# Optimization experiments

Hardware: AMD Instinct MI355X
Metric: run time of the kernel (lower is better)

The kernel has to match this reference:

```python
import jax, jax.numpy as jnp
import numpy as np

B, T, C = 4, 2048, 2048
N_HEAD = 16
HEAD_DIM = C // N_HEAD
ROPE_BASE = 10000.0


def setup_inputs() -> dict:
    key = jax.random.key(0)
    k1, k2, k3 = jax.random.split(key, 3)
    x = jax.random.normal(k1, (B, T, C), dtype=jnp.float32)
    Wqkv = jax.random.normal(k2, (C, 3 * C), dtype=jnp.float32) * 0.02
    bqkv = jnp.zeros((3 * C,), dtype=jnp.float32)
    Wproj = jax.random.normal(k3, (C, C), dtype=jnp.float32) * 0.02
    bproj = jnp.zeros((C,), dtype=jnp.float32)
    return {"x": x, "Wqkv": Wqkv, "bqkv": bqkv, "Wproj": Wproj, "bproj": bproj}


def _rope_cos_sin(seq_len, head_dim, dtype):
    inv_freq = 1.0 / (ROPE_BASE ** (jnp.arange(0, head_dim, 2, dtype=jnp.float32) / head_dim))
    t = jnp.arange(seq_len, dtype=jnp.float32)
    freqs = jnp.einsum("i,j->ij", t, inv_freq)          # [T, D/2]
    emb = jnp.concatenate([freqs, freqs], axis=-1)       # [T, D]
    return jnp.cos(emb).astype(dtype), jnp.sin(emb).astype(dtype)


def _rotate_half(x):
    half = x.shape[-1] // 2
    x1, x2 = x[..., :half], x[..., half:]
    return jnp.concatenate([-x2, x1], axis=-1)


def reference(x, Wqkv, bqkv, Wproj, bproj):
    b, t, c = x.shape
    qkv = x @ Wqkv + bqkv                                # [B, T, 3C]
    q, k, v = jnp.split(qkv, 3, axis=-1)
    # [B, T, C] -> [B, H, T, D]
    def to_heads(u):
        return u.reshape(b, t, N_HEAD, HEAD_DIM).transpose(0, 2, 1, 3)
    q, k, v = to_heads(q), to_heads(k), to_heads(v)
    cos, sin = _rope_cos_sin(t, HEAD_DIM, x.dtype)       # [T, D]
    cos = cos[None, None]                                # [1, 1, T, D]
    sin = sin[None, None]
    q = q * cos + _rotate_half(q) * sin
    k = k * cos + _rotate_half(k) * sin
    scale = 1.0 / np.sqrt(HEAD_DIM).astype(np.float32)
    scores = jnp.einsum("bhqd,bhkd->bhqk", q, k) * scale  # [B, H, T, T]
    causal = jnp.tril(jnp.ones((t, t), dtype=bool))
    scores = jnp.where(causal[None, None], scores, jnp.finfo(scores.dtype).min)
    att = jax.nn.softmax(scores, axis=-1)
    y = jnp.einsum("bhqk,bhkd->bhqd", att, v)             # [B, H, T, D]
    y = y.transpose(0, 2, 1, 3).reshape(b, t, c)
    return y @ Wproj + bproj
```

## Files before the change

### kernel.cpp

```cpp
#include <hip/hip_runtime.h>
#include <hip/hip_bf16.h>
#include <stdint.h>
#include <math.h>

#define NB 4
#define NT 2048
#define NC 2048
#define NH 16
#define HD 128
#define BT (NB*NT)

typedef __attribute__((ext_vector_type(8))) short s16x8;
typedef __attribute__((ext_vector_type(4))) short s16x4;
typedef __attribute__((ext_vector_type(4))) float f32x4;

typedef __attribute__((address_space(1))) void as1_void;
typedef __attribute__((address_space(3))) void as3_void;

static __device__ __forceinline__ unsigned short f2bf(float f) {
  union { float f; uint32_t u; } v; v.f = f;
  return (unsigned short)((v.u + 0x7fffu + ((v.u >> 16) & 1u)) >> 16);
}
static __device__ __forceinline__ float bf2f(unsigned short u) {
  union { uint32_t u; float f; } v; v.u = ((uint32_t)u) << 16;
  return v.f;
}
static __device__ __forceinline__ void async16(unsigned short* lds, const unsigned short* g) {
  __builtin_amdgcn_global_load_lds((as1_void*)g, (as3_void*)lds, 16, 0, 0);
}
static __device__ __forceinline__ uint32_t lds_off(void* p) {
  return (uint32_t)(size_t)(as3_void*)p;
}

__global__ void k_convert_bf16(const float* __restrict__ in, unsigned short* __restrict__ out, int n8) {
  int i = blockIdx.x * blockDim.x + threadIdx.x;
  if (i >= n8) return;
  const float4* p = (const float4*)in + (size_t)i * 2;
  float4 a = p[0], b = p[1];
  union { unsigned short s[8]; uint4 u; } o;
  o.s[0] = f2bf(a.x); o.s[1] = f2bf(a.y); o.s[2] = f2bf(a.z); o.s[3] = f2bf(a.w);
  o.s[4] = f2bf(b.x); o.s[5] = f2bf(b.y); o.s[6] = f2bf(b.z); o.s[7] = f2bf(b.w);
  ((uint4*)out)[i] = o.u;
}

__global__ void k_transpose_bf16(const float* __restrict__ W, unsigned short* __restrict__ WT, int K, int N) {
  __shared__ unsigned short tile[64][65];
  const int k0 = blockIdx.y * 64, n0 = blockIdx.x * 64;
  const int t = threadIdx.x;
  const int jj = t & 63, base_i = t >> 6;
  #pragma unroll
  for (int p = 0; p < 16; ++p) {
    int i = p * 4 + base_i;
    tile[i][jj] = f2bf(W[(size_t)(k0 + i) * N + n0 + jj]);
  }
  __syncthreads();
  #pragma unroll
  for (int p = 0; p < 16; ++p) {
    int j = p * 4 + base_i;
    WT[(size_t)(n0 + j) * K + k0 + jj] = tile[jj][j];
  }
}

__global__ void k_rope(unsigned short* __restrict__ Q, unsigned short* __restrict__ Kb) {
  int idx = blockIdx.x * 256 + threadIdx.x;
  int d = idx & 63;
  int tpos = (idx >> 6) & (NT - 1);
  int bh = idx >> 17;
  size_t o = ((size_t)bh * NT + tpos) * HD + d;
  float invf = exp2f(-(float)d * 0.2076205059304602f);
  float ang = (float)tpos * invf;
  float s, c;
  __sincosf(ang, &s, &c);
  float q1 = bf2f(Q[o]),  q2 = bf2f(Q[o + 64]);
  float k1 = bf2f(Kb[o]), k2 = bf2f(Kb[o + 64]);
  const float qs = 0.08838834764831845f * 1.4426950408889634f;
  Q[o]       = f2bf((q1 * c - q2 * s) * qs);
  Q[o + 64]  = f2bf((q2 * c + q1 * s) * qs);
  Kb[o]      = f2bf(k1 * c - k2 * s);
  Kb[o + 64] = f2bf(k2 * c + k1 * s);
}

template<int MODE>
__global__ __launch_bounds__(256, 2)
void k_gemm_bt2(const unsigned short* __restrict__ A,
                const unsigned short* __restrict__ Bt,
                const float* __restrict__ bias,
                float* __restrict__ OutF,
                unsigned short* __restrict__ Qd,
                unsigned short* __restrict__ Kd,
                unsigned short* __restrict__ Vd,
                int M, int N, int K)
{
  __shared__ __align__(16) unsigned short Al[256 * 64];
  __shared__ __align__(16) unsigned short Bl[128 * 64];
  const int t = threadIdx.x;
  const int l = t & 63;
  const int wv = t >> 6;
  const int wm = wv >> 1, wn = wv & 1;
  const int bm = blockIdx.y * 256, bn = blockIdx.x * 128;
  const int lr = l & 15, lg = l >> 4;

  f32x4 acc[8][4];
  #pragma unroll
  for (int i = 0; i < 8; ++i)
    #pragma unroll
    for (int j = 0; j < 4; ++j)
      acc[i][j] = f32x4{0.f, 0.f, 0.f, 0.f};

  for (int k0 = 0; k0 < K; k0 += 64) {
    #pragma unroll
    for (int i = 0; i < 8; ++i) {
      const int Cc = i * 256 + t;
      const int row = Cc >> 3;
      const int kc = (Cc & 7) ^ (row & 7);
      async16(&Al[(i * 256 + (t & 192)) * 8], &A[(size_t)(bm + row) * K + k0 + kc * 8]);
    }
    #pragma unroll
    for (int i = 0; i < 4; ++i) {
      const int Cc = i * 256 + t;
      const int row = Cc >> 3;
      const int kc = (Cc & 7) ^ (row & 7);
      async16(&Bl[(i * 256 + (t & 192)) * 8], &Bt[(size_t)(bn + row) * K + k0 + kc * 8]);
    }
    __syncthreads();
    #pragma unroll
    for (int kk = 0; kk < 2; ++kk) {
      s16x8 af[8], bfr[4];
      #pragma unroll
      for (int mi = 0; mi < 8; ++mi) {
        const int row = wm * 128 + mi * 16 + lr;
        const int ch = (kk * 4 + lg) ^ (row & 7);
        af[mi] = *(const s16x8*)&Al[row * 64 + ch * 8];
      }
      #pragma unroll
      for (int ni = 0; ni < 4; ++ni) {
        const int row = wn * 64 + ni * 16 + lr;
        const int ch = (kk * 4 + lg) ^ (row & 7);
        bfr[ni] = *(const s16x8*)&Bl[row * 64 + ch * 8];
      }
      __builtin_amdgcn_s_setprio(1);
      #pragma unroll
      for (int mi = 0; mi < 8; ++mi)
        #pragma unroll
        for (int ni = 0; ni < 4; ++ni)
          acc[mi][ni] = __builtin_amdgcn_mfma_f32_16x16x32_bf16(af[mi], bfr[ni], acc[mi][ni], 0, 0, 0);
      __builtin_amdgcn_s_setprio(0);
    }
    __syncthreads();
  }

  #pragma unroll
  for (int mi = 0; mi < 8; ++mi) {
    #pragma unroll
    for (int ni = 0; ni < 4; ++ni) {
      const int col = bn + wn * 64 + ni * 16 + lr;
      const float bv = bias[col];
      #pragma unroll
      for (int r = 0; r < 4; ++r) {
        const int row = bm + wm * 128 + mi * 16 + lg * 4 + r;
        const float v = acc[mi][ni][r] + bv;
        if (MODE == 1) {
          OutF[(size_t)row * N + col] = v;
        } else {
          const int which = col >> 11;
          const int cc = col & 2047;
          const int h = cc >> 7, d = cc & 127;
          const int b = row >> 11, tp = row & 2047;
          unsigned short* dst = (which == 0) ? Qd : (which == 1 ? Kd : Vd);
          dst[(((size_t)(b * NH + h)) * NT + tp) * HD + d] = f2bf(v);
        }
      }
    }
  }
}

__global__ __launch_bounds__(256, 2)
void k_attn(const unsigned short* __restrict__ Q,
            const unsigned short* __restrict__ Kg,
            const unsigned short* __restrict__ Vg,
            unsigned short* __restrict__ Yatt)
{
  __shared__ __align__(16) unsigned short Kl[2][64 * 128];
  __shared__ __align__(16) unsigned short Vl[2][64 * 128];
  const int bh = blockIdx.x;
  const int pair = blockIdx.y;
  const int b = bh >> 4, h = bh & 15;
  const int t = threadIdx.x, l = t & 63, wv = t >> 6;
  const int lr = l & 15, lg = l >> 4;
  const size_t hoff = (size_t)bh * NT * HD;
  const unsigned short* Qh = Q + hoff;
  const unsigned short* Kh = Kg + hoff;
  const unsigned short* Vh = Vg + hoff;
  const uint32_t vbase0 = lds_off(&Vl[0][0]);

  auto stageKV = [&](int buf, int kv0) {
    #pragma unroll
    for (int i = 0; i < 4; ++i) {
      const int Cc = i * 256 + t;
      {
        const int krow = Cc >> 4;
        const int kc = (Cc & 15) ^ (krow & 7);
        async16(&Kl[buf][(i * 256 + (t & 192)) * 8], &Kh[(size_t)(kv0 + krow) * HD + kc * 8]);
      }
      {
        const int S = Cc >> 3, c8 = Cc & 7;
        const int kq = S >> 3, dq = S & 7;
        const int vk = kq * 4 + (c8 >> 1), vd = dq * 16 + (c8 & 1) * 8;
        async16(&Vl[buf][(i * 256 + (t & 192)) * 8], &Vh[(size_t)(kv0 + vk) * HD + vd]);
      }
    }
  };

  #pragma unroll 1
  for (int rep = 0; rep < 2; ++rep) {
    const int qb = rep ? (31 - pair) : pair;
    const int q0w = qb * 64 + wv * 16;
    const int qrow = q0w + lr;

    __syncthreads();

    s16x8 qf[4];
    #pragma unroll
    for (int m = 0; m < 4; ++m)
      qf[m] = *(const s16x8*)(Qh + (size_t)qrow * HD + m * 32 + lg * 8);

    f32x4 yt[8];
    #pragma unroll
    for (int n = 0; n < 8; ++n) yt[n] = f32x4{0.f, 0.f, 0.f, 0.f};
    float mrun = -1e30f, lrun = 0.f;

    auto computeTile = [&](int buf, int kv0) {
      f32x4 st[4];
      __builtin_amdgcn_s_setprio(1);
      #pragma unroll
      for (int kt = 0; kt < 4; ++kt) {
        f32x4 a = f32x4{0.f, 0.f, 0.f, 0.f};
        const int krow = kt * 16 + lr;
        #pragma unroll
        for (int m = 0; m < 4; ++m) {
          const int ch = (m * 4 + lg) ^ (krow & 7);
          s16x8 kf = *(const s16x8*)&Kl[buf][krow * 128 + ch * 8];
          a = __builtin_amdgcn_mfma_f32_16x16x32_bf16(kf, qf[m], a, 0, 0, 0);
        }
        st[kt] = a;
      }
      __builtin_amdgcn_s_setprio(0);

      if (kv0 + 63 > q0w) {
        #pragma unroll
        for (int kt = 0; kt < 4; ++kt)
          #pragma unroll
          for (int r = 0; r < 4; ++r) {
            const int key = kv0 + kt * 16 + lg * 4 + r;
            if (key > qrow) st[kt][r] = -3.0e38f;
          }
      }

      float tm = -3.0e38f;
      #pragma unroll
      for (int kt = 0; kt < 4; ++kt)
        #pragma unroll
        for (int r = 0; r < 4; ++r) tm = fmaxf(tm, st[kt][r]);
      tm = fmaxf(tm, __shfl_xor(tm, 16));
      tm = fmaxf(tm, __shfl_xor(tm, 32));
      const float mnew = fmaxf(mrun, tm);
      const float fsc = exp2f(mrun - mnew);
      mrun = mnew;
      lrun *= fsc;
      #pragma unroll
      for (int n = 0; n < 8; ++n)
        #pragma unroll
        for (int r = 0; r < 4; ++r) yt[n][r] *= fsc;

      unsigned short pb[16];
      float psum = 0.f;
      #pragma unroll
      for (int kt = 0; kt < 4; ++kt)
        #pragma unroll
        for (int r = 0; r < 4; ++r) {
          const float p = exp2f(st[kt][r] - mnew);
          psum += p;
          pb[kt * 4 + r] = f2bf(p);
        }
      lrun += psum;

      s16x8 pf[2];
      #pragma unroll
      for (int gk = 0; gk < 2; ++gk)
        #pragma unroll
        for (int j = 0; j < 8; ++j)
          pf[gk][j] = (short)pb[(gk * 2 + (j >> 2)) * 4 + (j & 3)];

      const uint32_t vb = vbase0 + (uint32_t)buf * 16384;
      #pragma unroll
      for (int gk = 0; gk < 2; ++gk) {
        s16x4 va[8], vb2[8];
        #pragma unroll
        for (int n = 0; n < 8; ++n) {
          const uint32_t a0 = vb + ((uint32_t)((gk * 8 + lg) * 8 + n)) * 128 + (uint32_t)lr * 8;
          asm volatile("ds_read_b64_tr_b16 %0, %1" : "=v"(va[n])  : "v"(a0));
          asm volatile("ds_read_b64_tr_b16 %0, %1" : "=v"(vb2[n]) : "v"(a0 + 4096));
        }
        asm volatile("s_waitcnt lgkmcnt(0)" ::: "memory");
        __builtin_amdgcn_sched_barrier(0);
        __builtin_amdgcn_s_setprio(1);
        #pragma unroll
        for (int n = 0; n < 8; ++n) {
          s16x8 vf;
          vf[0] = va[n][0];  vf[1] = va[n][1];  vf[2] = va[n][2];  vf[3] = va[n][3];
          vf[4] = vb2[n][0]; vf[5] = vb2[n][1]; vf[6] = vb2[n][2]; vf[7] = vb2[n][3];
          yt[n] = __builtin_amdgcn_mfma_f32_16x16x32_bf16(vf, pf[gk], yt[n], 0, 0, 0);
        }
        __builtin_amdgcn_s_setprio(0);
      }
    };

    const int nkv = qb + 1;
    stageKV(0, 0);
    asm volatile("s_waitcnt vmcnt(0)" ::: "memory");
    __syncthreads();
    int buf = 0;
    #pragma unroll 1
    for (int kv = 0; kv < nkv - 1; ++kv) {
      stageKV(buf ^ 1, (kv + 1) * 64);
      computeTile(buf, kv * 64);
      asm volatile("s_waitcnt vmcnt(0)" ::: "memory");
      __builtin_amdgcn_s_barrier();
      buf ^= 1;
    }
    computeTile(buf, (nkv - 1) * 64);

    lrun += __shfl_xor(lrun, 16);
    lrun += __shfl_xor(lrun, 32);
    const float inv = 1.f / lrun;
    unsigned short* yrow = Yatt + (size_t)(b * NT + q0w + lr) * NC + h * HD;
    #pragma unroll
    for (int n = 0; n < 8; ++n)
      #pragma unroll
      for (int r = 0; r < 4; ++r)
        yrow[n * 16 + lg * 4 + r] = f2bf(yt[n][r] * inv);
  }
}

extern "C" void kernel_launch(void* const* d_in, const int* in_sizes, int n_in,
                              void* d_out, int out_size, void* d_ws, size_t ws_size,
                              hipStream_t stream) {
  (void)in_sizes; (void)n_in; (void)out_size; (void)ws_size;
  const float* x     = (const float*)d_in[0];
  const float* Wqkv  = (const float*)d_in[1];
  const float* bqkv  = (const float*)d_in[2];
  const float* Wproj = (const float*)d_in[3];
  const float* bproj = (const float*)d_in[4];
  float* out = (float*)d_out;
  char* ws = (char*)d_ws;

  unsigned short* xb     = (unsigned short*)(ws);
  unsigned short* WqkvT  = (unsigned short*)(ws + 33554432);
  unsigned short* WprojT = (unsigned short*)(ws + 58720256);
  unsigned short* Qb     = (unsigned short*)(ws + 67108864);
  unsigned short* Kb     = (unsigned short*)(ws + 100663296);
  unsigned short* Vb     = (unsigned short*)(ws + 134217728);
  unsigned short* att    = xb;

  k_convert_bf16<<<dim3(8192), dim3(256), 0, stream>>>(x, xb, BT * NC / 8);
  k_transpose_bf16<<<dim3(96, 32), dim3(256), 0, stream>>>(Wqkv, WqkvT, NC, 3 * NC);
  k_transpose_bf16<<<dim3(32, 32), dim3(256), 0, stream>>>(Wproj, WprojT, NC, NC);
  k_gemm_bt2<0><<<dim3(48, 32), dim3(256), 0, stream>>>(xb, WqkvT, bqkv, nullptr, Qb, Kb, Vb, BT, 3 * NC, NC);
  k_rope<<<dim3(32768), dim3(256), 0, stream>>>(Qb, Kb);
  k_attn<<<dim3(64, 16), dim3(256), 0, stream>>>(Qb, Kb, Vb, att);
  k_gemm_bt2<1><<<dim3(16, 32), dim3(256), 0, stream>>>(att, WprojT, bproj, out, nullptr, nullptr, nullptr, BT, NC, NC);
}
```

Baseline: 446.8 us.

## Vectorize RoPE loads, add lazy softmax rescale, use packed bf16 convert

The RoPE kernel now has each thread handle eight elements with 16-byte vector loads and stores, and the grid shrinks to match. In attention, the running-max rescale of the accumulator is skipped unless some lane's tile max exceeds the current max by more than 8 (log2 domain). This lets probabilities grow up to 2^8 before renormalising, which is still exact after the final division. Probabilities are packed to bf16 with the hardware v_cvt_pk_bf16_f32 instruction instead of software rounding, so rounding behaviour may differ slightly.

Measured after the change: 438.3 us. No clear change (-1.9%).

```diff
diff --git a/kernel.cpp b/kernel.cpp
--- a/kernel.cpp
+++ b/kernel.cpp
@@ -63,21 +63,32 @@
 
 __global__ void k_rope(unsigned short* __restrict__ Q, unsigned short* __restrict__ Kb) {
   int idx = blockIdx.x * 256 + threadIdx.x;
-  int d = idx & 63;
-  int tpos = (idx >> 6) & (NT - 1);
-  int bh = idx >> 17;
-  size_t o = ((size_t)bh * NT + tpos) * HD + d;
-  float invf = exp2f(-(float)d * 0.2076205059304602f);
-  float ang = (float)tpos * invf;
-  float s, c;
-  __sincosf(ang, &s, &c);
-  float q1 = bf2f(Q[o]),  q2 = bf2f(Q[o + 64]);
-  float k1 = bf2f(Kb[o]), k2 = bf2f(Kb[o + 64]);
+  int g = idx & 7;
+  int tpos = (idx >> 3) & (NT - 1);
+  int bh = idx >> 14;
+  size_t o = ((size_t)bh * NT + tpos) * HD + g * 8;
+  s16x8 qlo = *(const s16x8*)(Q + o),  qhi = *(const s16x8*)(Q + o + 64);
+  s16x8 klo = *(const s16x8*)(Kb + o), khi = *(const s16x8*)(Kb + o + 64);
+  s16x8 oql, oqh, okl, okh;
   const float qs = 0.08838834764831845f * 1.4426950408889634f;
-  Q[o]       = f2bf((q1 * c - q2 * s) * qs);
-  Q[o + 64]  = f2bf((q2 * c + q1 * s) * qs);
-  Kb[o]      = f2bf(k1 * c - k2 * s);
-  Kb[o + 64] = f2bf(k2 * c + k1 * s);
+  #pragma unroll
+  for (int e = 0; e < 8; ++e) {
+    const int d = g * 8 + e;
+    float invf = exp2f(-(float)d * 0.2076205059304602f);
+    float ang = (float)tpos * invf;
+    float s, c;
+    __sincosf(ang, &s, &c);
+    float q1 = bf2f((unsigned short)qlo[e]), q2 = bf2f((unsigned short)qhi[e]);
+    float k1 = bf2f((unsigned short)klo[e]), k2 = bf2f((unsigned short)khi[e]);
+    oql[e] = (short)f2bf((q1 * c - q2 * s) * qs);
+    oqh[e] = (short)f2bf((q2 * c + q1 * s) * qs);
+    okl[e] = (short)f2bf(k1 * c - k2 * s);
+    okh[e] = (short)f2bf(k2 * c + k1 * s);
+  }
+  *(s16x8*)(Q + o)       = oql;
+  *(s16x8*)(Q + o + 64)  = oqh;
+  *(s16x8*)(Kb + o)      = okl;
+  *(s16x8*)(Kb + o + 64) = okh;
 }
 
 template<int MODE>
@@ -263,33 +274,37 @@
         for (int r = 0; r < 4; ++r) tm = fmaxf(tm, st[kt][r]);
       tm = fmaxf(tm, __shfl_xor(tm, 16));
       tm = fmaxf(tm, __shfl_xor(tm, 32));
-      const float mnew = fmaxf(mrun, tm);
-      const float fsc = exp2f(mrun - mnew);
-      mrun = mnew;
-      lrun *= fsc;
-      #pragma unroll
-      for (int n = 0; n < 8; ++n)
-        #pragma unroll
-        for (int r = 0; r < 4; ++r) yt[n][r] *= fsc;
-
-      unsigned short pb[16];
+      if (!__all(tm - mrun <= 8.0f)) {
+        const float mnew = fmaxf(mrun, tm);
+        const float fsc = exp2f(mrun - mnew);
+        mrun = mnew;
+        lrun *= fsc;
+        #pragma unroll
+        for (int n = 0; n < 8; ++n)
+          #pragma unroll
+          for (int r = 0; r < 4; ++r) yt[n][r] *= fsc;
+      }
+
+      float pv[16];
       float psum = 0.f;
       #pragma unroll
       for (int kt = 0; kt < 4; ++kt)
         #pragma unroll
         for (int r = 0; r < 4; ++r) {
-          const float p = exp2f(st[kt][r] - mnew);
+          const float p = exp2f(st[kt][r] - mrun);
           psum += p;
-          pb[kt * 4 + r] = f2bf(p);
+          pv[kt * 4 + r] = p;
         }
       lrun += psum;
 
-      s16x8 pf[2];
+      union { uint32_t w[4]; s16x8 v; } pu[2];
       #pragma unroll
       for (int gk = 0; gk < 2; ++gk)
         #pragma unroll
-        for (int j = 0; j < 8; ++j)
-          pf[gk][j] = (short)pb[(gk * 2 + (j >> 2)) * 4 + (j & 3)];
+        for (int w = 0; w < 4; ++w) {
+          const int i0 = (gk * 2 + (w >> 1)) * 4 + (w & 1) * 2;
+          asm("v_cvt_pk_bf16_f32 %0, %1, %2" : "=v"(pu[gk].w[w]) : "v"(pv[i0]), "v"(pv[i0 + 1]));
+        }
 
       const uint32_t vb = vbase0 + (uint32_t)buf * 16384;
       #pragma unroll
@@ -309,7 +324,7 @@
           s16x8 vf;
           vf[0] = va[n][0];  vf[1] = va[n][1];  vf[2] = va[n][2];  vf[3] = va[n][3];
           vf[4] = vb2[n][0]; vf[5] = vb2[n][1]; vf[6] = vb2[n][2]; vf[7] = vb2[n][3];
-          yt[n] = __builtin_amdgcn_mfma_f32_16x16x32_bf16(vf, pf[gk], yt[n], 0, 0, 0);
+          yt[n] = __builtin_amdgcn_mfma_f32_16x16x32_bf16(vf, pu[gk].v, yt[n], 0, 0, 0);
         }
         __builtin_amdgcn_s_setprio(0);
       }
@@ -366,7 +381,7 @@
   k_transpose_bf16<<<dim3(96, 32), dim3(256), 0, stream>>>(Wqkv, WqkvT, NC, 3 * NC);
   k_transpose_bf16<<<dim3(32, 32), dim3(256), 0, stream>>>(Wproj, WprojT, NC, NC);
   k_gemm_bt2<0><<<dim3(48, 32), dim3(256), 0, stream>>>(xb, WqkvT, bqkv, nullptr, Qb, Kb, Vb, BT, 3 * NC, NC);
-  k_rope<<<dim3(32768), dim3(256), 0, stream>>>(Qb, Kb);
+  k_rope<<<dim3(4096), dim3(256), 0, stream>>>(Qb, Kb);
   k_attn<<<dim3(64, 16), dim3(256), 0, stream>>>(Qb, Kb, Vb, att);
   k_gemm_bt2<1><<<dim3(16, 32), dim3(256), 0, stream>>>(att, WprojT, bproj, out, nullptr, nullptr, nullptr, BT, NC, NC);
 }
```
